# Optimization experiments

Measured on AMD Instinct MI355X. Metric: run time of the kernel, lower is better.

The kernel has to match this reference:

```python
import jax, jax.numpy as jnp
import numpy as np

NUM_EMBEDDINGS = 1024
EMBEDDING_DIM = 256


def setup_inputs() -> dict:
    key = jax.random.key(0)
    k1, k2 = jax.random.split(key)
    z_e = jax.random.normal(k1, (32, EMBEDDING_DIM, 32, 32), dtype=jnp.float32)
    codebook = jax.random.normal(k2, (NUM_EMBEDDINGS, EMBEDDING_DIM), dtype=jnp.float32)
    return {"z_e": z_e, "codebook": codebook}


def reference(z_e, codebook):
    # z_e: [B, C, H, W] with C == embedding_dim; codebook: [K, C]
    B, C, H, W = z_e.shape
    K = codebook.shape[0]
    # _flatten: NCHW -> NHWC -> [N, C]
    z_nhwc = jnp.transpose(z_e, (0, 2, 3, 1))
    z_flat = z_nhwc.reshape(-1, C)
    # _compute_distances: ||z||^2 + ||e||^2 - 2 z e^T  -> [N, K]
    z_sq = jnp.sum(z_flat * z_flat, axis=1, keepdims=True)
    e_sq = jnp.sum(codebook * codebook, axis=1)
    distances = z_sq + e_sq - 2.0 * jnp.matmul(z_flat, codebook.T)
    # argmin + one-hot scatter (_build_encodings)
    indices = jnp.argmin(distances, axis=1)
    encodings = jax.nn.one_hot(indices, K, dtype=z_flat.dtype)  # [N, K]
    # _compute_perplexity
    avg_probs = jnp.mean(encodings, axis=0)
    perplexity = jnp.exp(-jnp.sum(avg_probs * jnp.log(avg_probs + 1e-10)))
    return distances, indices, encodings, perplexity
```

## Files before the change

### kernel.cpp

```cpp
#include <hip/hip_runtime.h>
#include <math.h>

#define N_ROWS 32768
#define K_CODES 1024
#define C_DIM 256
#define HW 1024

#define OFF_DIST 0
#define OFF_IDX  (N_ROWS * K_CODES)
#define OFF_ENC  (OFF_IDX + N_ROWS)
#define OFF_PERP (OFF_ENC + N_ROWS * K_CODES)

typedef __attribute__((ext_vector_type(8))) short short8;
typedef __attribute__((ext_vector_type(4))) float f32x4;

__device__ inline unsigned short bf16_rn(float x) {
    unsigned int u = __float_as_uint(x);
    unsigned int r = u + 0x7FFFu + ((u >> 16) & 1u);
    return (unsigned short)(r >> 16);
}
__device__ inline float bf16_to_f(unsigned short h) {
    return __uint_as_float(((unsigned int)h) << 16);
}

__device__ __forceinline__ void gl2lds16(const unsigned short* g, char* l) {
    __builtin_amdgcn_global_load_lds(
        (const __attribute__((address_space(1))) unsigned int*)g,
        (__attribute__((address_space(3))) unsigned int*)l, 16, 0, 0);
}

__global__ __launch_bounds__(256) void prep_kernel(
        const float* __restrict__ z, const float* __restrict__ cb,
        unsigned short* __restrict__ z_hi, unsigned short* __restrict__ z_lo,
        unsigned short* __restrict__ cb_hi, unsigned short* __restrict__ cb_lo,
        float* __restrict__ zsq, float* __restrict__ esq) {
    const int bid = blockIdx.x;
    const int t = threadIdx.x;

    if (bid >= 256) {
        const int lane = t & 63;
        const int k = (bid - 256) * 4 + (t >> 6);
        float4 v = *reinterpret_cast<const float4*>(cb + (size_t)k * C_DIM + lane * 4);
        float s = v.x * v.x + v.y * v.y + v.z * v.z + v.w * v.w;
        ushort4 h, l;
        h.x = bf16_rn(v.x); l.x = bf16_rn(v.x - bf16_to_f(h.x));
        h.y = bf16_rn(v.y); l.y = bf16_rn(v.y - bf16_to_f(h.y));
        h.z = bf16_rn(v.z); l.z = bf16_rn(v.z - bf16_to_f(h.z));
        h.w = bf16_rn(v.w); l.w = bf16_rn(v.w - bf16_to_f(h.w));
        *reinterpret_cast<ushort4*>(cb_hi + (size_t)k * C_DIM + lane * 4) = h;
        *reinterpret_cast<ushort4*>(cb_lo + (size_t)k * C_DIM + lane * 4) = l;
#pragma unroll
        for (int m = 1; m < 64; m <<= 1) s += __shfl_xor(s, m);
        if (lane == 0) esq[k] = s;
        return;
    }

    __shared__ float st[64][132];
    const int b = bid >> 3;
    const int hw0 = (bid & 7) * 128;

    const int c_r  = t >> 5;
    const int hw_r = (t & 31) * 4;
    const int hw_w = t >> 1;
    const int ch   = (t & 1) * 32;
    const int n    = b * HW + hw0 + hw_w;

    float zacc = 0.f;

    for (int c0 = 0; c0 < C_DIM; c0 += 64) {
#pragma unroll
        for (int it = 0; it < 8; ++it) {
            int c_l = it * 8 + c_r;
            float4 v = *reinterpret_cast<const float4*>(
                z + (size_t)b * (C_DIM * HW) + (size_t)(c0 + c_l) * HW + hw0 + hw_r);
            *reinterpret_cast<float4*>(&st[c_l][hw_r]) = v;
        }
        __syncthreads();

        short8 hv[4], lv[4];
#pragma unroll
        for (int j = 0; j < 32; ++j) {
            float x = st[ch + j][hw_w];
            unsigned short h = bf16_rn(x);
            unsigned short lo = bf16_rn(x - bf16_to_f(h));
            hv[j >> 3][j & 7] = (short)h;
            lv[j >> 3][j & 7] = (short)lo;
            zacc = fmaf(x, x, zacc);
        }
        unsigned short* hp = z_hi + (size_t)n * C_DIM + c0 + ch;
        unsigned short* lp = z_lo + (size_t)n * C_DIM + c0 + ch;
#pragma unroll
        for (int q = 0; q < 4; ++q) {
            *reinterpret_cast<short8*>(hp + q * 8) = hv[q];
            *reinterpret_cast<short8*>(lp + q * 8) = lv[q];
        }
        __syncthreads();
    }
    float o = __shfl_xor(zacc, 1);
    if ((t & 1) == 0) zsq[n] = zacc + o;
}

#define KSTEPS 24

__global__ __launch_bounds__(256) void dist_mfma_kernel(
        const unsigned short* __restrict__ z_hi,
        const unsigned short* __restrict__ z_lo,
        const unsigned short* __restrict__ cb_hi,
        const unsigned short* __restrict__ cb_lo,
        const float* __restrict__ zsq, const float* __restrict__ esq,
        float* __restrict__ dist, float2* __restrict__ partial) {
    __shared__ __align__(16) unsigned short As[2][128 * 32];
    __shared__ __align__(16) unsigned short Bs[2][128 * 32];
    __shared__ float2 pb[128][2];

    const int t = threadIdx.x;
    const int lane = t & 63, wid = t >> 6;
    const int wy = wid >> 1, wx = wid & 1;
    const int l15 = lane & 15, l4 = lane >> 4;

    const int kbi = blockIdx.x & 7;
    const int kb = kbi * 128;
    const int nb = (blockIdx.x >> 3) * 128;

#define STAGE(buf_, s_) do {                                                   \
        const int sp_ = (s_) >> 3;                                             \
        const int sc0_ = ((s_) & 7) * 32;                                      \
        const unsigned short* Ap_ = (sp_ == 2) ? z_lo : z_hi;                  \
        const unsigned short* Bp_ = (sp_ == 1) ? cb_lo : cb_hi;                \
        _Pragma("unroll")                                                      \
        for (int j_ = 0; j_ < 2; ++j_) {                                       \
            int ch_ = j_ * 256 + t;                                            \
            int row_ = ch_ >> 2, oct_ = ch_ & 3;                               \
            int lb_ = (j_ * 256 + (t & 192)) * 16;                             \
            gl2lds16(Ap_ + (size_t)(nb + row_) * C_DIM + sc0_ + oct_ * 8,      \
                     (char*)(&As[buf_][0]) + lb_);                             \
            gl2lds16(Bp_ + (size_t)(kb + row_) * C_DIM + sc0_ + oct_ * 8,      \
                     (char*)(&Bs[buf_][0]) + lb_);                             \
        }                                                                      \
    } while (0)

    f32x4 acc[4][4] = {};

    STAGE(0, 0);
    __syncthreads();

    for (int s = 0; s < KSTEPS; ++s) {
        const int cur = s & 1;
        if (s < KSTEPS - 1) STAGE(cur ^ 1, s + 1);

        short8 av[4], bv[4];
#pragma unroll
        for (int mi = 0; mi < 4; ++mi)
            av[mi] = *reinterpret_cast<const short8*>(
                &As[cur][(wy * 64 + mi * 16 + l15) * 32 + l4 * 8]);
#pragma unroll
        for (int ci = 0; ci < 4; ++ci)
            bv[ci] = *reinterpret_cast<const short8*>(
                &Bs[cur][(wx * 64 + ci * 16 + l15) * 32 + l4 * 8]);

#pragma unroll
        for (int mi = 0; mi < 4; ++mi)
#pragma unroll
            for (int ci = 0; ci < 4; ++ci)
                acc[mi][ci] = __builtin_amdgcn_mfma_f32_16x16x32_bf16(
                    av[mi], bv[ci], acc[mi][ci], 0, 0, 0);
        __syncthreads();
    }
#undef STAGE

    float zsv[4][4];
#pragma unroll
    for (int mi = 0; mi < 4; ++mi)
#pragma unroll
        for (int r = 0; r < 4; ++r)
            zsv[mi][r] = zsq[nb + wy * 64 + mi * 16 + l4 * 4 + r];
    float esv[4];
#pragma unroll
    for (int ci = 0; ci < 4; ++ci)
        esv[ci] = esq[kb + wx * 64 + ci * 16 + l15];

    float best[4][4];
    int bidx[4][4];
#pragma unroll
    for (int mi = 0; mi < 4; ++mi)
#pragma unroll
        for (int r = 0; r < 4; ++r) { best[mi][r] = 1e30f; bidx[mi][r] = K_CODES; }

#pragma unroll
    for (int mi = 0; mi < 4; ++mi) {
#pragma unroll
        for (int r = 0; r < 4; ++r) {
            int row = nb + wy * 64 + mi * 16 + l4 * 4 + r;
            float* drow = dist + (size_t)row * K_CODES;
#pragma unroll
            for (int ci = 0; ci < 4; ++ci) {
                int col = kb + wx * 64 + ci * 16 + l15;
                float d = zsv[mi][r] + esv[ci] - 2.f * acc[mi][ci][r];
                drow[col] = d;
                if (d < best[mi][r]) { best[mi][r] = d; bidx[mi][r] = col; }
            }
        }
    }

#pragma unroll
    for (int m = 1; m < 16; m <<= 1) {
#pragma unroll
        for (int mi = 0; mi < 4; ++mi)
#pragma unroll
            for (int r = 0; r < 4; ++r) {
                float ob = __shfl_xor(best[mi][r], m);
                int   oi = __shfl_xor(bidx[mi][r], m);
                if (ob < best[mi][r] || (ob == best[mi][r] && oi < bidx[mi][r])) {
                    best[mi][r] = ob; bidx[mi][r] = oi;
                }
            }
    }

    if (l15 == 0) {
#pragma unroll
        for (int mi = 0; mi < 4; ++mi)
#pragma unroll
            for (int r = 0; r < 4; ++r) {
                int rl = wy * 64 + mi * 16 + l4 * 4 + r;
                pb[rl][wx] = make_float2(best[mi][r], (float)bidx[mi][r]);
            }
    }
    __syncthreads();
    if (t < 128) {
        float2 a = pb[t][0], c = pb[t][1];
        float2 rr = (c.x < a.x) ? c : a;
        partial[(size_t)kbi * N_ROWS + nb + t] = rr;
    }
}

__global__ __launch_bounds__(256) void combenc_kernel(
        const float2* __restrict__ partial, float* __restrict__ idx_out,
        int* __restrict__ idx_int, float* __restrict__ enc) {
    __shared__ int sidx[16];
    const int t = threadIdx.x;
    const int r0 = blockIdx.x * 16;
    if (t < 16) {
        int n = r0 + t;
        float2 bv = partial[n];
#pragma unroll
        for (int kb = 1; kb < 8; ++kb) {
            float2 c = partial[(size_t)kb * N_ROWS + n];
            if (c.x < bv.x) bv = c;
        }
        idx_out[n] = bv.y;
        idx_int[n] = (int)bv.y;
        sidx[t] = (int)bv.y;
    }
    __syncthreads();
    const int k0 = t * 4;
#pragma unroll 4
    for (int r = 0; r < 16; ++r) {
        int bi = sidx[r];
        float4 v;
        v.x = (k0 + 0 == bi) ? 1.0f : 0.0f;
        v.y = (k0 + 1 == bi) ? 1.0f : 0.0f;
        v.z = (k0 + 2 == bi) ? 1.0f : 0.0f;
        v.w = (k0 + 3 == bi) ? 1.0f : 0.0f;
        *reinterpret_cast<float4*>(enc + (size_t)(r0 + r) * K_CODES + k0) = v;
    }
}

__global__ __launch_bounds__(1024) void perp_kernel(const int* __restrict__ idxi,
                                                    float* __restrict__ out) {
    __shared__ int hist[K_CODES];
    __shared__ float wsum[16];
    const int t = threadIdx.x;
    hist[t] = 0;
    __syncthreads();
    for (int n = t; n < N_ROWS; n += 1024)
        atomicAdd(&hist[idxi[n]], 1);
    __syncthreads();
    float p = (float)hist[t] * (1.0f / (float)N_ROWS);
    float s = p * logf(p + 1e-10f);
#pragma unroll
    for (int off = 32; off > 0; off >>= 1) s += __shfl_down(s, off);
    if ((t & 63) == 0) wsum[t >> 6] = s;
    __syncthreads();
    if (t == 0) {
        float tot = 0.f;
#pragma unroll
        for (int w = 0; w < 16; ++w) tot += wsum[w];
        out[0] = expf(-tot);
    }
}

extern "C" void kernel_launch(void* const* d_in, const int* in_sizes, int n_in,
                              void* d_out, int out_size, void* d_ws, size_t ws_size,
                              hipStream_t stream) {
    const float* z  = (const float*)d_in[0];
    const float* cb = (const float*)d_in[1];
    float* out  = (float*)d_out;
    float* dist = out + OFF_DIST;
    float* idxo = out + OFF_IDX;
    float* enc  = out + OFF_ENC;
    float* perp = out + OFF_PERP;

    char* wsb = (char*)d_ws;
    float*  zsq  = (float*)(wsb + 0);
    float*  esq  = (float*)(wsb + 131072);
    int*    idxi = (int*)(wsb + 135168);
    float2* part = (float2*)(wsb + 266240);

    unsigned short* z_hi  = (unsigned short*)enc;
    unsigned short* z_lo  = z_hi + (size_t)N_ROWS * C_DIM;
    unsigned short* cb_hi = z_lo + (size_t)N_ROWS * C_DIM;
    unsigned short* cb_lo = cb_hi + (size_t)K_CODES * C_DIM;

    prep_kernel<<<512, 256, 0, stream>>>(z, cb, z_hi, z_lo, cb_hi, cb_lo, zsq, esq);
    dist_mfma_kernel<<<2048, 256, 0, stream>>>(z_hi, z_lo, cb_hi, cb_lo,
                                               zsq, esq, dist, part);
    combenc_kernel<<<N_ROWS / 16, 256, 0, stream>>>(part, idxo, idxi, enc);
    perp_kernel<<<1, 1024, 0, stream>>>(idxi, perp);
}
```

Measured before the change: 442.3 us.

## Widen distance GEMM tile to 128x256 with 8 waves and swizzled block order

The distance kernel now uses 512-thread blocks with a 2x4 wave layout. Each block covers 256 codebook columns instead of 128, so each staged A tile is reused across twice as many codes and the block count halves. Block indices are remapped (swizzled) so that neighbouring blocks share row tiles, which may improve L2 locality. The per-row argmin reduction now merges 4 waves, and the cross-block combine reduces over 4 partials instead of 8. LDS use and per-block register pressure rise, which could lower occupancy.

```diff
diff --git a/kernel.cpp b/kernel.cpp
--- a/kernel.cpp
+++ b/kernel.cpp
@@ -102,7 +102,7 @@
 
 #define KSTEPS 24
 
-__global__ __launch_bounds__(256) void dist_mfma_kernel(
+__global__ __launch_bounds__(512) void dist_mfma_kernel(
         const unsigned short* __restrict__ z_hi,
         const unsigned short* __restrict__ z_lo,
         const unsigned short* __restrict__ cb_hi,
@@ -110,33 +110,31 @@
         const float* __restrict__ zsq, const float* __restrict__ esq,
         float* __restrict__ dist, float2* __restrict__ partial) {
     __shared__ __align__(16) unsigned short As[2][128 * 32];
-    __shared__ __align__(16) unsigned short Bs[2][128 * 32];
-    __shared__ float2 pb[128][2];
+    __shared__ __align__(16) unsigned short Bs[2][256 * 32];
+    __shared__ float2 pb[128][4];
 
     const int t = threadIdx.x;
     const int lane = t & 63, wid = t >> 6;
-    const int wy = wid >> 1, wx = wid & 1;
+    const int wy = wid >> 2, wx = wid & 3;
     const int l15 = lane & 15, l4 = lane >> 4;
 
-    const int kbi = blockIdx.x & 7;
-    const int kb = kbi * 128;
-    const int nb = (blockIdx.x >> 3) * 128;
+    const int swz = (blockIdx.x & 7) * 128 + (blockIdx.x >> 3);
+    const int kbi = swz & 3;
+    const int kb = kbi * 256;
+    const int nb = (swz >> 2) * 128;
 
 #define STAGE(buf_, s_) do {                                                   \
         const int sp_ = (s_) >> 3;                                             \
         const int sc0_ = ((s_) & 7) * 32;                                      \
         const unsigned short* Ap_ = (sp_ == 2) ? z_lo : z_hi;                  \
         const unsigned short* Bp_ = (sp_ == 1) ? cb_lo : cb_hi;                \
-        _Pragma("unroll")                                                      \
-        for (int j_ = 0; j_ < 2; ++j_) {                                       \
-            int ch_ = j_ * 256 + t;                                            \
-            int row_ = ch_ >> 2, oct_ = ch_ & 3;                               \
-            int lb_ = (j_ * 256 + (t & 192)) * 16;                             \
-            gl2lds16(Ap_ + (size_t)(nb + row_) * C_DIM + sc0_ + oct_ * 8,      \
-                     (char*)(&As[buf_][0]) + lb_);                             \
-            gl2lds16(Bp_ + (size_t)(kb + row_) * C_DIM + sc0_ + oct_ * 8,      \
-                     (char*)(&Bs[buf_][0]) + lb_);                             \
-        }                                                                      \
+        const int wb_ = (t & ~63) * 16;                                        \
+        gl2lds16(Ap_ + (size_t)(nb + (t >> 2)) * C_DIM + sc0_ + (t & 3) * 8,   \
+                 (char*)(&As[buf_][0]) + wb_);                                 \
+        gl2lds16(Bp_ + (size_t)(kb + (t >> 2)) * C_DIM + sc0_ + (t & 3) * 8,   \
+                 (char*)(&Bs[buf_][0]) + wb_);                                 \
+        gl2lds16(Bp_ + (size_t)(kb + 128 + (t >> 2)) * C_DIM + sc0_ + (t & 3) * 8, \
+                 (char*)(&Bs[buf_][0]) + 8192 + wb_);                          \
     } while (0)
 
     f32x4 acc[4][4] = {};
@@ -227,9 +225,13 @@
     }
     __syncthreads();
     if (t < 128) {
-        float2 a = pb[t][0], c = pb[t][1];
-        float2 rr = (c.x < a.x) ? c : a;
-        partial[(size_t)kbi * N_ROWS + nb + t] = rr;
+        float2 bv2 = pb[t][0];
+#pragma unroll
+        for (int w = 1; w < 4; ++w) {
+            float2 c = pb[t][w];
+            if (c.x < bv2.x) bv2 = c;
+        }
+        partial[(size_t)kbi * N_ROWS + nb + t] = bv2;
     }
 }
 
@@ -243,7 +245,7 @@
         int n = r0 + t;
         float2 bv = partial[n];
 #pragma unroll
-        for (int kb = 1; kb < 8; ++kb) {
+        for (int kb = 1; kb < 4; ++kb) {
             float2 c = partial[(size_t)kb * N_ROWS + n];
             if (c.x < bv.x) bv = c;
         }
@@ -312,7 +314,7 @@
     unsigned short* cb_lo = cb_hi + (size_t)K_CODES * C_DIM;
 
     prep_kernel<<<512, 256, 0, stream>>>(z, cb, z_hi, z_lo, cb_hi, cb_lo, zsq, esq);
-    dist_mfma_kernel<<<2048, 256, 0, stream>>>(z_hi, z_lo, cb_hi, cb_lo,
+    dist_mfma_kernel<<<1024, 512, 0, stream>>>(z_hi, z_lo, cb_hi, cb_lo,
                                                zsq, esq, dist, part);
     combenc_kernel<<<N_ROWS / 16, 256, 0, stream>>>(part, idxo, idxi, enc);
     perp_kernel<<<1, 1024, 0, stream>>>(idxi, perp);
```

Result: faster. 390.1 us (-11.8%).
